# Kernel optimization log

Measured on AMD Instinct MI355X. Metric: run time of the kernel, lower is better.

Reference implementation:

```python
import jax, jax.numpy as jnp
import numpy as np

E = 1024      # embed_dim
H = 16        # num_heads
D = E // H    # head_dim = 64
K = 4         # num_hyper_nodes
MAX_SEQ = 8192
ROPE_BASE = 10000.0
SCALE = D ** -0.5


def rotate_half(x):
    half = x.shape[-1] // 2
    return jnp.concatenate([-x[..., half:], x[..., :half]], axis=-1)


def _rope_cache():
    inv_freq = 1.0 / (ROPE_BASE ** (jnp.arange(0, D, 2, dtype=jnp.float32) / D))
    t = jnp.arange(MAX_SEQ, dtype=jnp.float32)
    freqs = jnp.outer(t, inv_freq)                       # (MAX_SEQ, D/2)
    emb = jnp.concatenate([freqs, freqs], axis=-1)       # (MAX_SEQ, D)
    return jnp.cos(emb), jnp.sin(emb)


def setup_inputs() -> dict:
    key = jax.random.key(0)
    ks = jax.random.split(key, 6)
    B, S = 2, 2048
    w_scale = E ** -0.5  # keep pre-softmax logits in a sane range
    return {
        "x":  jax.random.normal(ks[0], (B, S, E), dtype=jnp.float32),
        "Wq": jax.random.normal(ks[1], (E, E), dtype=jnp.float32) * w_scale,
        "Wk": jax.random.normal(ks[2], (E, E), dtype=jnp.float32) * w_scale,
        "Wv": jax.random.normal(ks[3], (E, E), dtype=jnp.float32) * w_scale,
        "Wr": jax.random.normal(ks[4], (E, H * K), dtype=jnp.float32) * w_scale,
        "Wo": jax.random.normal(ks[5], (E, E), dtype=jnp.float32) * w_scale,
    }


def reference(x, Wq, Wk, Wv, Wr, Wo):
    B, S, _ = x.shape
    # projections -> (B, H, S, D)
    q = (x @ Wq).reshape(B, S, H, D).transpose(0, 2, 1, 3)
    k = (x @ Wk).reshape(B, S, H, D).transpose(0, 2, 1, 3)
    v = (x @ Wv).reshape(B, S, H, D).transpose(0, 2, 1, 3)

    # node routing probabilities (B, H, S, K)
    logits = (x @ Wr).reshape(B, S, H, K).transpose(0, 2, 1, 3)
    node_probs = jax.nn.softmax(logits, axis=-1)

    # expected per-node position: sum_{j<i} p[j,k]  -> (B, H, S, K)
    expected_pos = jnp.cumsum(node_probs, axis=2) - node_probs

    # fractional-position RoPE via linear interpolation of the cos/sin cache
    cos_c, sin_c = _rope_cache()
    pos = jnp.clip(expected_pos, 0.0, MAX_SEQ - 1)
    pf = pos.astype(jnp.int32)                   # floor
    pc = jnp.minimum(pf + 1, MAX_SEQ - 1)        # ceil
    frac = (pos - pf.astype(pos.dtype))[..., None]
    cos = cos_c[pf] + frac * (cos_c[pc] - cos_c[pf])   # (B,H,S,K,D)
    sin = sin_c[pf] + frac * (sin_c[pc] - sin_c[pf])

    # Weighted combine over nodes. Since q_k = q*cos_k + rh(q)*sin_k is linear
    # in (cos_k, sin_k), sum_k p_k * q_k = q * (sum_k p_k cos_k) + rh(q) * (sum_k p_k sin_k)
    cos_w = jnp.einsum('bhsk,bhskd->bhsd', node_probs, cos)
    sin_w = jnp.einsum('bhsk,bhskd->bhsd', node_probs, sin)
    q_r = q * cos_w + rotate_half(q) * sin_w
    k_r = k * cos_w + rotate_half(k) * sin_w

    # P(same node) weights (B, H, S, S)
    node_w = jnp.einsum('bhik,bhjk->bhij', node_probs, node_probs)

    scores = jnp.einsum('bhid,bhjd->bhij', q_r, k_r) * SCALE
    scores = scores + jnp.log(node_w + 1e-8)
    causal = jnp.tril(jnp.ones((S, S), dtype=bool))
    scores = jnp.where(causal[None, None], scores, -jnp.inf)
    attn = jax.nn.softmax(scores, axis=-1)

    out = jnp.einsum('bhij,bhjd->bhid', attn, v)
    out = out.transpose(0, 2, 1, 3).reshape(B, S, E)
    return out @ Wo
```

## Files before the change

### kernel.cpp

```cpp
#include <hip/hip_runtime.h>

#define E_ 1024
#define H_ 16
#define D_ 64
#define K_ 4
#define S_ 2048
#define B_ 2
#define BS_ 4096
#define BH_ 32
#define CT_ 2080

typedef __attribute__((ext_vector_type(8))) short short8;
typedef __attribute__((ext_vector_type(4))) float f32x4;
typedef __attribute__((ext_vector_type(4))) unsigned short u16x4;

__device__ __forceinline__ unsigned short f2bf(float f) {
  union { float f; unsigned u; } v; v.f = f;
  unsigned r = v.u + 0x7FFFu + ((v.u >> 16) & 1u);
  return (unsigned short)(r >> 16);
}
__device__ __forceinline__ float bf2f(unsigned short u) {
  union { unsigned u; float f; } v; v.u = ((unsigned)u) << 16; return v.f;
}

typedef __attribute__((address_space(1))) const void gvoid;
typedef __attribute__((address_space(3))) void lvoid;
__device__ __forceinline__ void gload_lds16(const void* g, void* l) {
  __builtin_amdgcn_global_load_lds((gvoid*)g, (lvoid*)l, 16, 0, 0);
}

__device__ __forceinline__ short8 lds8(const unsigned short* base, int row, int chunk) {
  int off = row * 128 + (((chunk ^ (row & 7)) & 7) << 4);
  return *(const short8*)((const char*)base + off);
}

#define SWZ_(d) (((d) & 7) ^ (((d) >> 3) & 7))

__global__ __launch_bounds__(256) void k_convert_x(const float* __restrict__ x,
                                                   unsigned short* __restrict__ xb) {
  int i = blockIdx.x * 256 + threadIdx.x;
  float4 v = ((const float4*)x)[i];
  u16x4 o; o.x = f2bf(v.x); o.y = f2bf(v.y); o.z = f2bf(v.z); o.w = f2bf(v.w);
  ((u16x4*)xb)[i] = o;
}

__global__ __launch_bounds__(256) void k_transpose_w(const float* __restrict__ Wq,
    const float* __restrict__ Wk, const float* __restrict__ Wv, const float* __restrict__ Wo,
    unsigned short* __restrict__ wt) {
  const float* W = blockIdx.z == 0 ? Wq : blockIdx.z == 1 ? Wk : blockIdx.z == 2 ? Wv : Wo;
  unsigned short* out = wt + (size_t)blockIdx.z * E_ * E_;
  __shared__ float tile[64][65];
  int k0 = blockIdx.y * 64, n0 = blockIdx.x * 64;
  int r = threadIdx.x >> 2, q4 = threadIdx.x & 3;
#pragma unroll
  for (int q = 0; q < 4; q++) {
    int c4 = q4 + q * 4;
    float4 v = *(const float4*)&W[(size_t)(k0 + r) * E_ + n0 + c4 * 4];
    tile[r][c4 * 4 + 0] = v.x; tile[r][c4 * 4 + 1] = v.y;
    tile[r][c4 * 4 + 2] = v.z; tile[r][c4 * 4 + 3] = v.w;
  }
  __syncthreads();
#pragma unroll
  for (int q = 0; q < 4; q++) {
    int cb = (q4 + q * 4) * 4;
    u16x4 o;
    o.x = f2bf(tile[cb + 0][r]); o.y = f2bf(tile[cb + 1][r]);
    o.z = f2bf(tile[cb + 2][r]); o.w = f2bf(tile[cb + 3][r]);
    *(u16x4*)&out[(size_t)(n0 + r) * E_ + k0 + cb] = o;
  }
}

__global__ __launch_bounds__(256) void k_cache(float* __restrict__ cosc, float* __restrict__ sinc) {
  int i = blockIdx.x * 256 + threadIdx.x;
  if (i >= CT_ * 32) return;
  int tt = i >> 5, f = i & 31;
  float invf = __expf(-(float)(2 * f) * (9.210340371976184f / 64.f));
  float ang = (float)tt * invf;
  cosc[i] = cosf(ang); sinc[i] = sinf(ang);
}

__global__ __launch_bounds__(256) void k_router(const float* __restrict__ x,
    const float* __restrict__ Wr, float* __restrict__ logits) {
  int rowblk = blockIdx.x * 8;
  int c = threadIdx.x & 63, rg = threadIdx.x >> 6;
  __shared__ float xs[8][128];
  float acc0 = 0.f, acc1 = 0.f;
  for (int e0 = 0; e0 < E_; e0 += 128) {
    __syncthreads();
    int idx = threadIdx.x;
    float4 v = *(const float4*)&x[(size_t)(rowblk + (idx >> 5)) * E_ + e0 + (idx & 31) * 4];
    *(float4*)&xs[idx >> 5][(idx & 31) * 4] = v;
    __syncthreads();
#pragma unroll 8
    for (int e = 0; e < 128; e++) {
      float w = Wr[(size_t)(e0 + e) * 64 + c];
      acc0 = fmaf(xs[rg * 2 + 0][e], w, acc0);
      acc1 = fmaf(xs[rg * 2 + 1][e], w, acc1);
    }
  }
  logits[(size_t)(rowblk + rg * 2 + 0) * 64 + c] = acc0;
  logits[(size_t)(rowblk + rg * 2 + 1) * 64 + c] = acc1;
}

__global__ __launch_bounds__(256) void k_scan(const float* __restrict__ logits,
    float* __restrict__ probs, unsigned short* __restrict__ pb, float* __restrict__ epos) {
  int bh = blockIdx.x; int b = bh >> 4, h = bh & 15;
  int t = threadIdx.x;
  float p[8][4];
  float own[4] = {0.f, 0.f, 0.f, 0.f};
#pragma unroll
  for (int r = 0; r < 8; r++) {
    int s = t * 8 + r;
    float4 lg = *(const float4*)&logits[(size_t)(b * S_ + s) * 64 + h * 4];
    float m = fmaxf(fmaxf(lg.x, lg.y), fmaxf(lg.z, lg.w));
    float e0 = __expf(lg.x - m), e1 = __expf(lg.y - m), e2 = __expf(lg.z - m), e3 = __expf(lg.w - m);
    float inv = 1.f / (e0 + e1 + e2 + e3);
    p[r][0] = e0 * inv; p[r][1] = e1 * inv; p[r][2] = e2 * inv; p[r][3] = e3 * inv;
    own[0] += p[r][0]; own[1] += p[r][1]; own[2] += p[r][2]; own[3] += p[r][3];
    float4 pv; pv.x = p[r][0]; pv.y = p[r][1]; pv.z = p[r][2]; pv.w = p[r][3];
    *(float4*)&probs[((size_t)bh * S_ + s) * 4] = pv;
    u16x4 pu; pu.x = f2bf(p[r][0]); pu.y = f2bf(p[r][1]);
    pu.z = f2bf(p[r][2]); pu.w = f2bf(p[r][3]);
    *(u16x4*)&pb[((size_t)bh * S_ + s) * 4] = pu;
  }
  __shared__ float sc[4][256];
#pragma unroll
  for (int k = 0; k < 4; k++) sc[k][t] = own[k];
  __syncthreads();
  for (int off = 1; off < 256; off <<= 1) {
    float v0 = 0, v1 = 0, v2 = 0, v3 = 0;
    if (t >= off) { v0 = sc[0][t - off]; v1 = sc[1][t - off]; v2 = sc[2][t - off]; v3 = sc[3][t - off]; }
    __syncthreads();
    if (t >= off) { sc[0][t] += v0; sc[1][t] += v1; sc[2][t] += v2; sc[3][t] += v3; }
    __syncthreads();
  }
  float run[4];
#pragma unroll
  for (int k = 0; k < 4; k++) run[k] = sc[k][t] - own[k];
#pragma unroll
  for (int r = 0; r < 8; r++) {
    int s = t * 8 + r;
    float4 ev; ev.x = run[0]; ev.y = run[1]; ev.z = run[2]; ev.w = run[3];
    *(float4*)&epos[((size_t)bh * S_ + s) * 4] = ev;
    run[0] += p[r][0]; run[1] += p[r][1]; run[2] += p[r][2]; run[3] += p[r][3];
  }
}

__global__ __launch_bounds__(256) void k_cwsw(const float* __restrict__ probs,
    const float* __restrict__ epos, const float* __restrict__ cosc, const float* __restrict__ sinc,
    float* __restrict__ cw, float* __restrict__ sw) {
  int bh = blockIdx.y;
  int s = blockIdx.x * 8 + (threadIdx.x >> 5);
  int f = threadIdx.x & 31;
  size_t row = (size_t)bh * S_ + s;
  float cacc = 0.f, sacc = 0.f;
#pragma unroll
  for (int k = 0; k < 4; k++) {
    float pk = probs[row * 4 + k];
    float pos = epos[row * 4 + k];
    pos = fminf(fmaxf(pos, 0.f), (float)(CT_ - 2));
    int pf = (int)pos; float fr = pos - (float)pf;
    float c0 = cosc[pf * 32 + f], c1 = cosc[pf * 32 + 32 + f];
    float s0 = sinc[pf * 32 + f], s1 = sinc[pf * 32 + 32 + f];
    cacc = fmaf(pk, c0 + fr * (c1 - c0), cacc);
    sacc = fmaf(pk, s0 + fr * (s1 - s0), sacc);
  }
  cw[row * 32 + f] = cacc; sw[row * 32 + f] = sacc;
}

__device__ __forceinline__ void gemm_128x128(const unsigned short* __restrict__ A,
    const unsigned short* __restrict__ Bt, int m0, int n0,
    unsigned short* lA, unsigned short* lB, f32x4 acc[4][4]) {
  int t = threadIdx.x, w = t >> 6, lane = t & 63;
  int wm = w >> 1, wn = w & 1;
  int arow = lane & 15, agrp = lane >> 4;
  for (int k0 = 0; k0 < E_; k0 += 64) {
    __syncthreads();
#pragma unroll
    for (int j = 0; j < 4; j++) {
      int c = j * 256 + w * 64 + lane;
      int row = c >> 3, slot = c & 7;
      gload_lds16(A + (size_t)(m0 + row) * E_ + k0 + ((slot ^ (row & 7)) << 3),
                  lA + (size_t)(j * 256 + w * 64) * 8);
      gload_lds16(Bt + (size_t)(n0 + row) * E_ + k0 + ((slot ^ (row & 7)) << 3),
                  lB + (size_t)(j * 256 + w * 64) * 8);
    }
    __syncthreads();
#pragma unroll
    for (int ks = 0; ks < 2; ks++) {
      short8 af[4], bfr[4];
#pragma unroll
      for (int mi = 0; mi < 4; mi++) af[mi] = lds8(lA, wm * 64 + mi * 16 + arow, ks * 4 + agrp);
#pragma unroll
      for (int nj = 0; nj < 4; nj++) bfr[nj] = lds8(lB, wn * 64 + nj * 16 + arow, ks * 4 + agrp);
#pragma unroll
      for (int mi = 0; mi < 4; mi++)
#pragma unroll
        for (int nj = 0; nj < 4; nj++)
          acc[mi][nj] = __builtin_amdgcn_mfma_f32_16x16x32_bf16(af[mi], bfr[nj], acc[mi][nj], 0, 0, 0);
    }
  }
}

__global__ __launch_bounds__(256) void k_gemm_qkv(const unsigned short* __restrict__ xb,
    const unsigned short* __restrict__ wt, const float* __restrict__ cw, const float* __restrict__ sw,
    unsigned short* __restrict__ qr, unsigned short* __restrict__ kr, unsigned short* __restrict__ vb) {
  __shared__ unsigned short lA[128 * 64], lB[128 * 64];
  int z = blockIdx.z;
  int m0 = blockIdx.y * 128, n0 = blockIdx.x * 128;
  f32x4 acc[4][4];
  f32x4 zero4 = {0.f, 0.f, 0.f, 0.f};
#pragma unroll
  for (int a = 0; a < 4; a++)
#pragma unroll
    for (int b2 = 0; b2 < 4; b2++) acc[a][b2] = zero4;
  gemm_128x128(xb, wt + (size_t)z * E_ * E_, m0, n0, lA, lB, acc);

  int t = threadIdx.x, w = t >> 6, lane = t & 63;
  int wm = w >> 1, wn = w & 1;
  int arow = lane & 15, agrp = lane >> 4;
  if (z == 2) {
#pragma unroll
    for (int mi = 0; mi < 4; mi++)
#pragma unroll
      for (int reg = 0; reg < 4; reg++) {
        int i = m0 + wm * 64 + mi * 16 + agrp * 4 + reg;
        int b = i >> 11, s = i & 2047;
#pragma unroll
        for (int nj = 0; nj < 4; nj++) {
          int col = n0 + wn * 64 + nj * 16 + arow;
          int h = col >> 6, d = col & 63;
          vb[((size_t)(b * H_ + h) * S_ + s) * 64 + d] = f2bf(acc[mi][nj][reg]);
        }
      }
  } else {
    unsigned short* out = (z == 0) ? qr : kr;
    float scl = (z == 0) ? 0.125f : 1.0f;
    int h = (n0 + wn * 64) >> 6;
#pragma unroll
    for (int mi = 0; mi < 4; mi++)
#pragma unroll
      for (int reg = 0; reg < 4; reg++) {
        int i = m0 + wm * 64 + mi * 16 + agrp * 4 + reg;
        int b = i >> 11, s = i & 2047;
        size_t rbase = (size_t)(b * H_ + h) * S_ + s;
        float cw0 = cw[rbase * 32 + arow], cw1 = cw[rbase * 32 + 16 + arow];
        float sw0 = sw[rbase * 32 + arow], sw1 = sw[rbase * 32 + 16 + arow];
#pragma unroll
        for (int nj = 0; nj < 4; nj++) {
          float v = acc[mi][nj][reg];
          float part = acc[mi][nj ^ 2][reg];
          float rh = (nj < 2) ? -part : part;
          float cwv = (nj & 1) ? cw1 : cw0;
          float swv = (nj & 1) ? sw1 : sw0;
          out[rbase * 64 + nj * 16 + arow] = f2bf((v * cwv + rh * swv) * scl);
        }
      }
  }
}

__global__ __launch_bounds__(256) void k_gemm_out(const unsigned short* __restrict__ ob,
    const unsigned short* __restrict__ wot, float* __restrict__ dout) {
  __shared__ unsigned short lA[64 * 64];
  __shared__ unsigned short lB[128 * 64];
  int m0 = blockIdx.y * 64, n0 = blockIdx.x * 128;
  int t = threadIdx.x, w = t >> 6, lane = t & 63;
  int arow = lane & 15, agrp = lane >> 4;
  f32x4 acc[4][2];
  f32x4 zero4 = {0.f, 0.f, 0.f, 0.f};
#pragma unroll
  for (int a = 0; a < 4; a++) { acc[a][0] = zero4; acc[a][1] = zero4; }
  for (int k0 = 0; k0 < E_; k0 += 64) {
    __syncthreads();
#pragma unroll
    for (int j = 0; j < 2; j++) {
      int c = j * 256 + t;
      int row = c >> 3, slot = c & 7;
      gload_lds16(ob + (size_t)(m0 + row) * E_ + k0 + ((slot ^ (row & 7)) << 3),
                  lA + (size_t)c * 8);
    }
#pragma unroll
    for (int j = 0; j < 4; j++) {
      int c = j * 256 + t;
      int row = c >> 3, slot = c & 7;
      gload_lds16(wot + (size_t)(n0 + row) * E_ + k0 + ((slot ^ (row & 7)) << 3),
                  lB + (size_t)c * 8);
    }
    __syncthreads();
#pragma unroll
    for (int ks = 0; ks < 2; ks++) {
      short8 af[4], bfr[2];
#pragma unroll
      for (int mi = 0; mi < 4; mi++) af[mi] = lds8(lA, mi * 16 + arow, ks * 4 + agrp);
#pragma unroll
      for (int nj = 0; nj < 2; nj++) bfr[nj] = lds8(lB, w * 32 + nj * 16 + arow, ks * 4 + agrp);
#pragma unroll
      for (int mi = 0; mi < 4; mi++)
#pragma unroll
        for (int nj = 0; nj < 2; nj++)
          acc[mi][nj] = __builtin_amdgcn_mfma_f32_16x16x32_bf16(af[mi], bfr[nj], acc[mi][nj], 0, 0, 0);
    }
  }
#pragma unroll
  for (int mi = 0; mi < 4; mi++)
#pragma unroll
    for (int reg = 0; reg < 4; reg++) {
      int i = m0 + mi * 16 + agrp * 4 + reg;
#pragma unroll
      for (int nj = 0; nj < 2; nj++) {
        int col = n0 + w * 32 + nj * 16 + arow;
        dout[(size_t)i * E_ + col] = acc[mi][nj][reg];
      }
    }
}

__device__ const int4 kChunk[38] = {
  { 8,0, 8, 8},{ 8,9,17, 9},{12,0, 8,19},{12,9,17,20},
  { 7,0, 7, 6},{ 7,8,15, 7},{10,0, 7,13},{11,0, 7,16},{11,8,15,17},{11,16,23,18},
  {12,18,25,21},{14,0, 7,26},{14,8,15,27},{15,0, 7,30},{15,8,15,31},{15,16,23,32},
  {15,24,31,33},{ 3,0, 7,-1},
  { 6,0, 6, 4},{ 6,7,13, 5},{ 9,0, 6,10},{ 9,7,13,11},{10,8,14,14},{10,15,21,15},
  {13,0, 6,22},{13,7,13,23},{13,14,20,24},{13,21,27,25},{14,16,22,28},{14,23,29,29},
  { 5,0, 5, 2},{ 5,6,11, 3},{ 9,14,19,12},{ 2,0, 5,-1},
  { 4,0, 4, 0},{ 4,5, 9, 1},{ 1,0, 3,-1},{ 0,0, 1,-1}
};

__device__ __forceinline__ void attn_half(
    const unsigned short* lK, unsigned short* lPh,
    const short8 piF, const short8 pjF[4],
    int kv0, int ig_base, int arow, int agrp,
    const short8 qf[2],
    float mrow[4], float lrow[4], f32x4 oacc[4]) {
  f32x4 zero4 = {0.f, 0.f, 0.f, 0.f};
  f32x4 eps4 = {1e-8f, 1e-8f, 1e-8f, 1e-8f};
  f32x4 sacc[4], nwa[4];
#pragma unroll
  for (int ct = 0; ct < 4; ct++) {
    sacc[ct] = zero4;
    nwa[ct] = __builtin_amdgcn_mfma_f32_16x16x32_bf16(piF, pjF[ct], eps4, 0, 0, 0);
  }
#pragma unroll
  for (int ks = 0; ks < 2; ks++) {
#pragma unroll
    for (int ct = 0; ct < 4; ct++) {
      short8 kf = lds8(lK, ct * 16 + arow, ks * 4 + agrp);
      sacc[ct] = __builtin_amdgcn_mfma_f32_16x16x32_bf16(qf[ks], kf, sacc[ct], 0, 0, 0);
    }
  }
  float sv[4][4];
  float rmax[4] = {-1e30f, -1e30f, -1e30f, -1e30f};
#pragma unroll
  for (int ct = 0; ct < 4; ct++) {
    int jg = kv0 + ct * 16 + arow;
#pragma unroll
    for (int reg = 0; reg < 4; reg++) {
      int ig = ig_base + agrp * 4 + reg;
      float xv = sacc[ct][reg];
      if (jg > ig) xv = -1e30f;
      sv[ct][reg] = xv;
      rmax[reg] = fmaxf(rmax[reg], xv);
    }
  }
#pragma unroll
  for (int reg = 0; reg < 4; reg++) {
    rmax[reg] = fmaxf(rmax[reg], __shfl_xor(rmax[reg], 1, 16));
    rmax[reg] = fmaxf(rmax[reg], __shfl_xor(rmax[reg], 2, 16));
    rmax[reg] = fmaxf(rmax[reg], __shfl_xor(rmax[reg], 4, 16));
    rmax[reg] = fmaxf(rmax[reg], __shfl_xor(rmax[reg], 8, 16));
  }
  float alpha[4], rsum[4];
#pragma unroll
  for (int reg = 0; reg < 4; reg++) {
    float mn = fmaxf(mrow[reg], rmax[reg]);
    alpha[reg] = __expf(mrow[reg] - mn);
    mrow[reg] = mn; rsum[reg] = 0.f;
  }
#pragma unroll
  for (int ct = 0; ct < 4; ct++)
#pragma unroll
    for (int reg = 0; reg < 4; reg++) {
      float p = __expf(sv[ct][reg] - mrow[reg]) * nwa[ct][reg];
      sv[ct][reg] = p; rsum[reg] += p;
    }
#pragma unroll
  for (int reg = 0; reg < 4; reg++) {
    rsum[reg] += __shfl_xor(rsum[reg], 1, 16);
    rsum[reg] += __shfl_xor(rsum[reg], 2, 16);
    rsum[reg] += __shfl_xor(rsum[reg], 4, 16);
    rsum[reg] += __shfl_xor(rsum[reg], 8, 16);
    lrow[reg] = lrow[reg] * alpha[reg] + rsum[reg];
  }
#pragma unroll
  for (int dt = 0; dt < 4; dt++) {
    f32x4 o = oacc[dt];
    o.x *= alpha[0]; o.y *= alpha[1]; o.z *= alpha[2]; o.w *= alpha[3];
    oacc[dt] = o;
  }
#pragma unroll
  for (int ct = 0; ct < 4; ct++)
#pragma unroll
    for (int reg = 0; reg < 4; reg++) {
      int row = agrp * 4 + reg, col = ct * 16 + arow;
      int off = row * 128 + ((col * 2) ^ ((row & 7) << 4));
      *(unsigned short*)((char*)lPh + off) = f2bf(sv[ct][reg]);
    }
}

__device__ __forceinline__ void attn_pv(const unsigned short* lPh, const unsigned short* lV,
    int arow, int agrp, f32x4 oacc[4]) {
#pragma unroll
  for (int ks = 0; ks < 2; ks++) {
    short8 pf8 = lds8(lPh, arow, ks * 4 + agrp);
#pragma unroll
    for (int dt = 0; dt < 4; dt++) {
      int d = dt * 16 + arow;
      int off = d * 128 + ((((ks * 4 + agrp)) ^ SWZ_(d)) << 4);
      short8 vf = *(const short8*)((char*)lV + off);
      oacc[dt] = __builtin_amdgcn_mfma_f32_16x16x32_bf16(pf8, vf, oacc[dt], 0, 0, 0);
    }
  }
}

__global__ __launch_bounds__(256, 2) void k_attn(const unsigned short* __restrict__ qr,
    const unsigned short* __restrict__ kr, const unsigned short* __restrict__ vb,
    const unsigned short* __restrict__ pb, unsigned short* __restrict__ ob,
    unsigned short* __restrict__ ObP, float* __restrict__ ml) {
  __shared__ unsigned short lK[64 * 64];
  __shared__ unsigned short lV[64 * 64];
  __shared__ unsigned short lP[4][2][16 * 64];
  int4 ck = kChunk[blockIdx.x];
  int qt2 = ck.x, j0 = ck.y, j1 = ck.z, part = ck.w;
  int bh = blockIdx.y;
  int t = threadIdx.x, w = t >> 6, lane = t & 63;
  int arow = lane & 15, agrp = lane >> 4;
  int q0 = qt2 * 128;
  size_t base = (size_t)bh * S_ * 64;
  size_t bhS = (size_t)bh * S_;

  short8 qf[2][2];
  short8 piF[2];
  float mrow[2][4], lrow[2][4];
  f32x4 oacc[2][4];
  f32x4 zero4 = {0.f, 0.f, 0.f, 0.f};
#pragma unroll
  for (int hh = 0; hh < 2; hh++) {
#pragma unroll
    for (int ks = 0; ks < 2; ks++)
      qf[hh][ks] = *(const short8*)&qr[base + (size_t)(q0 + hh * 64 + w * 16 + arow) * 64 + ks * 32 + agrp * 8];
    short8 z = {0, 0, 0, 0, 0, 0, 0, 0};
    if (agrp == 0) {
      u16x4 pv = *(const u16x4*)&pb[(bhS + q0 + hh * 64 + w * 16 + arow) * 4];
      z[0] = (short)pv.x; z[1] = (short)pv.y; z[2] = (short)pv.z; z[3] = (short)pv.w;
    }
    piF[hh] = z;
#pragma unroll
    for (int reg = 0; reg < 4; reg++) { mrow[hh][reg] = -1e30f; lrow[hh][reg] = 0.f; }
#pragma unroll
    for (int dt = 0; dt < 4; dt++) oacc[hh][dt] = zero4;
  }

  for (int jt = j0; jt <= j1; jt++) {
    int kv0 = jt * 64;
    __syncthreads();
#pragma unroll
    for (int j = 0; j < 2; j++) {
      int c = j * 256 + w * 64 + lane;
      int row = c >> 3, slot = c & 7;
      gload_lds16(kr + base + (size_t)(kv0 + row) * 64 + ((slot ^ (row & 7)) << 3),
                  lK + (size_t)(j * 256 + w * 64) * 8);
    }
#pragma unroll
    for (int j = 0; j < 2; j++) {
      int c = j * 256 + t;
      int row = c >> 3; int d0 = (c & 7) * 8;
      short8 vv = *(const short8*)&vb[base + (size_t)(kv0 + row) * 64 + d0];
#pragma unroll
      for (int x = 0; x < 8; x++) {
        int d = d0 + x;
        int off = d * 128 + ((row * 2) ^ (SWZ_(d) << 4));
        *(unsigned short*)((char*)lV + off) = (unsigned short)vv[x];
      }
    }
    short8 pjF[4];
#pragma unroll
    for (int ct = 0; ct < 4; ct++) {
      short8 z = {0, 0, 0, 0, 0, 0, 0, 0};
      if (agrp == 0) {
        u16x4 pv = *(const u16x4*)&pb[(bhS + kv0 + ct * 16 + arow) * 4];
        z[0] = (short)pv.x; z[1] = (short)pv.y; z[2] = (short)pv.z; z[3] = (short)pv.w;
      }
      pjF[ct] = z;
    }
    __syncthreads();

    __builtin_amdgcn_s_setprio(1);
#pragma unroll
    for (int hh = 0; hh < 2; hh++)
      attn_half(lK, &lP[w][hh][0], piF[hh], pjF, kv0, q0 + hh * 64 + w * 16, arow, agrp,
                qf[hh], mrow[hh], lrow[hh], oacc[hh]);
    __builtin_amdgcn_s_setprio(0);
    asm volatile("s_waitcnt lgkmcnt(0)" ::: "memory");
    __builtin_amdgcn_sched_barrier(0);
    __builtin_amdgcn_s_setprio(1);
#pragma unroll
    for (int hh = 0; hh < 2; hh++)
      attn_pv(&lP[w][hh][0], lV, arow, agrp, oacc[hh]);
    __builtin_amdgcn_s_setprio(0);
  }

  if (part >= 0) {
    unsigned short* Op = ObP + ((size_t)bh * 34 + part) * 8192;
    float* mlp = ml + ((size_t)bh * 34 + part) * 256;
#pragma unroll
    for (int hh = 0; hh < 2; hh++) {
#pragma unroll
      for (int dt = 0; dt < 4; dt++)
#pragma unroll
        for (int reg = 0; reg < 4; reg++) {
          int row = hh * 64 + w * 16 + agrp * 4 + reg;
          Op[row * 64 + dt * 16 + arow] = f2bf(oacc[hh][dt][reg]);
        }
      if (arow == 0) {
#pragma unroll
        for (int reg = 0; reg < 4; reg++) {
          int row = hh * 64 + w * 16 + agrp * 4 + reg;
          mlp[row] = mrow[hh][reg];
          mlp[128 + row] = lrow[hh][reg];
        }
      }
    }
  } else {
    int b = bh >> 4, h8 = bh & 15;
#pragma unroll
    for (int hh = 0; hh < 2; hh++)
#pragma unroll
      for (int dt = 0; dt < 4; dt++)
#pragma unroll
        for (int reg = 0; reg < 4; reg++) {
          int i = q0 + hh * 64 + w * 16 + agrp * 4 + reg;
          int d = dt * 16 + arow;
          float v = oacc[hh][dt][reg] / lrow[hh][reg];
          ob[((size_t)(b * S_ + i) * H_ + h8) * 64 + d] = f2bf(v);
        }
  }
}

__global__ __launch_bounds__(256) void k_merge(const unsigned short* __restrict__ ObP,
    const float* __restrict__ ml, unsigned short* __restrict__ ob) {
  int qx = blockIdx.x, bh = blockIdx.y;
  int qt2 = 4 + qx;
  int np = qt2 <= 8 ? 2 : (qt2 <= 12 ? 3 : 4);
  int bslot = qt2 <= 8 ? (qt2 - 4) * 2 : (qt2 <= 12 ? 10 + (qt2 - 9) * 3 : 22 + (qt2 - 13) * 4);
  int t = threadIdx.x;
  int r = t >> 1, dh = (t & 1) * 32;
  float mp[4], lp[4];
  float m = -1e30f;
  for (int p2 = 0; p2 < np; p2++) {
    const float* mlp = ml + ((size_t)bh * 34 + bslot + p2) * 256;
    mp[p2] = mlp[r]; lp[p2] = mlp[128 + r];
    m = fmaxf(m, mp[p2]);
  }
  float a[4], l = 0.f;
  for (int p2 = 0; p2 < np; p2++) { a[p2] = __expf(mp[p2] - m); l = fmaf(lp[p2], a[p2], l); }
  float inv = 1.f / l;
  for (int p2 = 0; p2 < np; p2++) a[p2] *= inv;
  int i = qt2 * 128 + r, b = bh >> 4, h = bh & 15;
  unsigned short* op = ob + ((size_t)(b * S_ + i) * H_ + h) * 64 + dh;
#pragma unroll
  for (int q = 0; q < 8; q++) {
    float a0 = 0.f, a1 = 0.f, a2 = 0.f, a3 = 0.f;
    for (int p2 = 0; p2 < np; p2++) {
      const unsigned short* Op = ObP + ((size_t)bh * 34 + bslot + p2) * 8192 + r * 64 + dh + q * 4;
      u16x4 xx = *(const u16x4*)Op;
      a0 = fmaf(bf2f(xx.x), a[p2], a0);
      a1 = fmaf(bf2f(xx.y), a[p2], a1);
      a2 = fmaf(bf2f(xx.z), a[p2], a2);
      a3 = fmaf(bf2f(xx.w), a[p2], a3);
    }
    u16x4 o; o.x = f2bf(a0); o.y = f2bf(a1); o.z = f2bf(a2); o.w = f2bf(a3);
    *(u16x4*)(op + q * 4) = o;
  }
}

extern "C" void kernel_launch(void* const* d_in, const int* in_sizes, int n_in,
                              void* d_out, int out_size, void* d_ws, size_t ws_size,
                              hipStream_t stream) {
  const float* x  = (const float*)d_in[0];
  const float* Wq = (const float*)d_in[1];
  const float* Wk = (const float*)d_in[2];
  const float* Wv = (const float*)d_in[3];
  const float* Wr = (const float*)d_in[4];
  const float* Wo = (const float*)d_in[5];
  float* dout = (float*)d_out;

  char* p = (char*)d_ws;
  auto alloc = [&](size_t bytes) -> char* {
    char* r = p; p += (bytes + 255) & ~(size_t)255; return r;
  };
  unsigned short* xb   = (unsigned short*)alloc((size_t)BS_ * E_ * 2);
  unsigned short* wt   = (unsigned short*)alloc((size_t)4 * E_ * E_ * 2);
  float* cosc          = (float*)alloc((size_t)CT_ * 32 * 4);
  float* sinc          = (float*)alloc((size_t)CT_ * 32 * 4);
  float* probs         = (float*)alloc((size_t)BH_ * S_ * 4 * 4);
  unsigned short* pb   = (unsigned short*)alloc((size_t)BH_ * S_ * 4 * 2);
  float* logits        = (float*)alloc((size_t)BS_ * 64 * 4);
  float* epos          = (float*)alloc((size_t)BH_ * S_ * 4 * 4);
  float* cw            = (float*)alloc((size_t)BH_ * S_ * 32 * 4);
  float* sw            = (float*)alloc((size_t)BH_ * S_ * 32 * 4);
  unsigned short* qrb  = (unsigned short*)alloc((size_t)BH_ * S_ * 64 * 2);
  unsigned short* krb  = (unsigned short*)alloc((size_t)BH_ * S_ * 64 * 2);
  unsigned short* vbb  = (unsigned short*)alloc((size_t)BH_ * S_ * 64 * 2);
  unsigned short* obb  = (unsigned short*)alloc((size_t)BS_ * E_ * 2);
  if ((size_t)(p - (char*)d_ws) > ws_size) return;

  unsigned short* ObP = (unsigned short*)logits;
  float* mlbuf = (float*)xb;

  k_convert_x<<<BS_ * E_ / 4 / 256, 256, 0, stream>>>(x, xb);
  k_transpose_w<<<dim3(16, 16, 4), 256, 0, stream>>>(Wq, Wk, Wv, Wo, wt);
  k_cache<<<(CT_ * 32 + 255) / 256, 256, 0, stream>>>(cosc, sinc);
  k_router<<<BS_ / 8, 256, 0, stream>>>(x, Wr, logits);
  k_scan<<<BH_, 256, 0, stream>>>(logits, probs, pb, epos);
  k_cwsw<<<dim3(S_ / 8, BH_), 256, 0, stream>>>(probs, epos, cosc, sinc, cw, sw);
  k_gemm_qkv<<<dim3(8, 32, 3), 256, 0, stream>>>(xb, wt, cw, sw, qrb, krb, vbb);
  k_attn<<<dim3(38, BH_), 256, 0, stream>>>(qrb, krb, vbb, pb, obb, ObP, mlbuf);
  k_merge<<<dim3(12, BH_), 256, 0, stream>>>(ObP, mlbuf, obb);
  k_gemm_out<<<dim3(8, 64), 256, 0, stream>>>(obb, wt + (size_t)3 * E_ * E_, dout);
}
```

Before: 230.6 us.

## Double-buffer K/V tiles in attention, use exp2 softmax, remap blocks per XCD

The attention kernel now double-buffers K and V in LDS and prefetches the next tile's K, V and routing probabilities while the current tile is processed. This leaves one barrier per iteration and overlaps global loads with MFMA work. The QK and PV MFMAs for both query halves are interleaved to share K/V fragment loads, and the causal mask is skipped on tiles that lie fully below the diagonal. Softmax switches to exp2 with log2(e) folded into the Q scale. The 2D grid is flattened and remapped so each XCD handles a fixed set of heads for L2 locality. These changes double LDS use and add register pressure, which may lower occupancy.

```diff
diff --git a/kernel.cpp b/kernel.cpp
--- a/kernel.cpp
+++ b/kernel.cpp
@@ -235,7 +235,7 @@
       }
   } else {
     unsigned short* out = (z == 0) ? qr : kr;
-    float scl = (z == 0) ? 0.125f : 1.0f;
+    float scl = (z == 0) ? 0.18033688011f : 1.0f;
     int h = (n0 + wn * 64) >> 6;
 #pragma unroll
     for (int mi = 0; mi < 4; mi++)
@@ -325,41 +325,50 @@
   { 4,0, 4, 0},{ 4,5, 9, 1},{ 1,0, 3,-1},{ 0,0, 1,-1}
 };
 
-__device__ __forceinline__ void attn_half(
-    const unsigned short* lK, unsigned short* lPh,
-    const short8 piF, const short8 pjF[4],
-    int kv0, int ig_base, int arow, int agrp,
-    const short8 qf[2],
+__device__ __forceinline__ void qk_phase(const unsigned short* lKc, const short8 qf[2][2],
+                                         int arow, int agrp, f32x4 sacc[2][4]) {
+#pragma unroll
+  for (int ks = 0; ks < 2; ks++)
+#pragma unroll
+    for (int ct = 0; ct < 4; ct++) {
+      short8 kf = lds8(lKc, ct * 16 + arow, ks * 4 + agrp);
+      sacc[0][ct] = __builtin_amdgcn_mfma_f32_16x16x32_bf16(qf[0][ks], kf, sacc[0][ct], 0, 0, 0);
+      sacc[1][ct] = __builtin_amdgcn_mfma_f32_16x16x32_bf16(qf[1][ks], kf, sacc[1][ct], 0, 0, 0);
+    }
+}
+
+__device__ __forceinline__ void softmax_half(const f32x4 sacc[4], const short8 piF,
+    const short8 pjF[4], unsigned short* lPh, int kv0, int ig_base, int arow, int agrp,
     float mrow[4], float lrow[4], f32x4 oacc[4]) {
-  f32x4 zero4 = {0.f, 0.f, 0.f, 0.f};
   f32x4 eps4 = {1e-8f, 1e-8f, 1e-8f, 1e-8f};
-  f32x4 sacc[4], nwa[4];
-#pragma unroll
-  for (int ct = 0; ct < 4; ct++) {
-    sacc[ct] = zero4;
+  f32x4 nwa[4];
+#pragma unroll
+  for (int ct = 0; ct < 4; ct++)
     nwa[ct] = __builtin_amdgcn_mfma_f32_16x16x32_bf16(piF, pjF[ct], eps4, 0, 0, 0);
-  }
-#pragma unroll
-  for (int ks = 0; ks < 2; ks++) {
-#pragma unroll
-    for (int ct = 0; ct < 4; ct++) {
-      short8 kf = lds8(lK, ct * 16 + arow, ks * 4 + agrp);
-      sacc[ct] = __builtin_amdgcn_mfma_f32_16x16x32_bf16(qf[ks], kf, sacc[ct], 0, 0, 0);
-    }
-  }
   float sv[4][4];
   float rmax[4] = {-1e30f, -1e30f, -1e30f, -1e30f};
-#pragma unroll
-  for (int ct = 0; ct < 4; ct++) {
-    int jg = kv0 + ct * 16 + arow;
-#pragma unroll
-    for (int reg = 0; reg < 4; reg++) {
-      int ig = ig_base + agrp * 4 + reg;
-      float xv = sacc[ct][reg];
-      if (jg > ig) xv = -1e30f;
-      sv[ct][reg] = xv;
-      rmax[reg] = fmaxf(rmax[reg], xv);
-    }
+  if (kv0 + 63 > ig_base) {
+#pragma unroll
+    for (int ct = 0; ct < 4; ct++) {
+      int jg = kv0 + ct * 16 + arow;
+#pragma unroll
+      for (int reg = 0; reg < 4; reg++) {
+        int ig = ig_base + agrp * 4 + reg;
+        float xv = sacc[ct][reg];
+        if (jg > ig) xv = -1e30f;
+        sv[ct][reg] = xv;
+        rmax[reg] = fmaxf(rmax[reg], xv);
+      }
+    }
+  } else {
+#pragma unroll
+    for (int ct = 0; ct < 4; ct++)
+#pragma unroll
+      for (int reg = 0; reg < 4; reg++) {
+        float xv = sacc[ct][reg];
+        sv[ct][reg] = xv;
+        rmax[reg] = fmaxf(rmax[reg], xv);
+      }
   }
 #pragma unroll
   for (int reg = 0; reg < 4; reg++) {
@@ -372,14 +381,14 @@
 #pragma unroll
   for (int reg = 0; reg < 4; reg++) {
     float mn = fmaxf(mrow[reg], rmax[reg]);
-    alpha[reg] = __expf(mrow[reg] - mn);
+    alpha[reg] = __builtin_amdgcn_exp2f(mrow[reg] - mn);
     mrow[reg] = mn; rsum[reg] = 0.f;
   }
 #pragma unroll
   for (int ct = 0; ct < 4; ct++)
 #pragma unroll
     for (int reg = 0; reg < 4; reg++) {
-      float p = __expf(sv[ct][reg] - mrow[reg]) * nwa[ct][reg];
+      float p = __builtin_amdgcn_exp2f(sv[ct][reg] - mrow[reg]) * nwa[ct][reg];
       sv[ct][reg] = p; rsum[reg] += p;
     }
 #pragma unroll
@@ -406,17 +415,19 @@
     }
 }
 
-__device__ __forceinline__ void attn_pv(const unsigned short* lPh, const unsigned short* lV,
-    int arow, int agrp, f32x4 oacc[4]) {
+__device__ __forceinline__ void pv_phase(const unsigned short* lP0, const unsigned short* lP1,
+    const unsigned short* lVc, int arow, int agrp, f32x4 oacc0[4], f32x4 oacc1[4]) {
 #pragma unroll
   for (int ks = 0; ks < 2; ks++) {
-    short8 pf8 = lds8(lPh, arow, ks * 4 + agrp);
+    short8 pf0 = lds8(lP0, arow, ks * 4 + agrp);
+    short8 pf1 = lds8(lP1, arow, ks * 4 + agrp);
 #pragma unroll
     for (int dt = 0; dt < 4; dt++) {
       int d = dt * 16 + arow;
       int off = d * 128 + ((((ks * 4 + agrp)) ^ SWZ_(d)) << 4);
-      short8 vf = *(const short8*)((char*)lV + off);
-      oacc[dt] = __builtin_amdgcn_mfma_f32_16x16x32_bf16(pf8, vf, oacc[dt], 0, 0, 0);
+      short8 vf = *(const short8*)((const char*)lVc + off);
+      oacc0[dt] = __builtin_amdgcn_mfma_f32_16x16x32_bf16(pf0, vf, oacc0[dt], 0, 0, 0);
+      oacc1[dt] = __builtin_amdgcn_mfma_f32_16x16x32_bf16(pf1, vf, oacc1[dt], 0, 0, 0);
     }
   }
 }
@@ -425,12 +436,14 @@
     const unsigned short* __restrict__ kr, const unsigned short* __restrict__ vb,
     const unsigned short* __restrict__ pb, unsigned short* __restrict__ ob,
     unsigned short* __restrict__ ObP, float* __restrict__ ml) {
-  __shared__ unsigned short lK[64 * 64];
-  __shared__ unsigned short lV[64 * 64];
+  __shared__ unsigned short lK[2][64 * 64];
+  __shared__ unsigned short lV[2][64 * 64];
   __shared__ unsigned short lP[4][2][16 * 64];
-  int4 ck = kChunk[blockIdx.x];
+  int id = blockIdx.x;
+  int xcd = id & 7, slt = id >> 3;
+  int bh = xcd * 4 + (slt & 3);
+  int4 ck = kChunk[slt >> 2];
   int qt2 = ck.x, j0 = ck.y, j1 = ck.z, part = ck.w;
-  int bh = blockIdx.y;
   int t = threadIdx.x, w = t >> 6, lane = t & 63;
   int arow = lane & 15, agrp = lane >> 4;
   int q0 = qt2 * 128;
@@ -447,11 +460,10 @@
 #pragma unroll
     for (int ks = 0; ks < 2; ks++)
       qf[hh][ks] = *(const short8*)&qr[base + (size_t)(q0 + hh * 64 + w * 16 + arow) * 64 + ks * 32 + agrp * 8];
+    u16x4 pv = {0, 0, 0, 0};
+    if (agrp == 0) pv = *(const u16x4*)&pb[(bhS + q0 + hh * 64 + w * 16 + arow) * 4];
     short8 z = {0, 0, 0, 0, 0, 0, 0, 0};
-    if (agrp == 0) {
-      u16x4 pv = *(const u16x4*)&pb[(bhS + q0 + hh * 64 + w * 16 + arow) * 4];
-      z[0] = (short)pv.x; z[1] = (short)pv.y; z[2] = (short)pv.z; z[3] = (short)pv.w;
-    }
+    z[0] = (short)pv.x; z[1] = (short)pv.y; z[2] = (short)pv.z; z[3] = (short)pv.w;
     piF[hh] = z;
 #pragma unroll
     for (int reg = 0; reg < 4; reg++) { mrow[hh][reg] = -1e30f; lrow[hh][reg] = 0.f; }
@@ -459,53 +471,101 @@
     for (int dt = 0; dt < 4; dt++) oacc[hh][dt] = zero4;
   }
 
-  for (int jt = j0; jt <= j1; jt++) {
-    int kv0 = jt * 64;
-    __syncthreads();
+  auto stageK = [&](int jt, int buf) {
 #pragma unroll
     for (int j = 0; j < 2; j++) {
       int c = j * 256 + w * 64 + lane;
       int row = c >> 3, slot = c & 7;
-      gload_lds16(kr + base + (size_t)(kv0 + row) * 64 + ((slot ^ (row & 7)) << 3),
-                  lK + (size_t)(j * 256 + w * 64) * 8);
-    }
+      gload_lds16(kr + base + (size_t)(jt * 64 + row) * 64 + ((slot ^ (row & 7)) << 3),
+                  &lK[buf][(size_t)(j * 256 + w * 64) * 8]);
+    }
+  };
+  auto loadV = [&](int jt, short8 vr[2]) {
 #pragma unroll
     for (int j = 0; j < 2; j++) {
       int c = j * 256 + t;
-      int row = c >> 3; int d0 = (c & 7) * 8;
-      short8 vv = *(const short8*)&vb[base + (size_t)(kv0 + row) * 64 + d0];
+      int row = c >> 3, d0 = (c & 7) * 8;
+      vr[j] = *(const short8*)&vb[base + (size_t)(jt * 64 + row) * 64 + d0];
+    }
+  };
+  auto scatterV = [&](const short8 vr[2], int buf) {
+#pragma unroll
+    for (int j = 0; j < 2; j++) {
+      int c = j * 256 + t;
+      int row = c >> 3, d0 = (c & 7) * 8;
 #pragma unroll
       for (int x = 0; x < 8; x++) {
         int d = d0 + x;
         int off = d * 128 + ((row * 2) ^ (SWZ_(d) << 4));
-        *(unsigned short*)((char*)lV + off) = (unsigned short)vv[x];
+        *(unsigned short*)((char*)&lV[buf][0] + off) = (unsigned short)vr[j][x];
       }
     }
+  };
+  auto loadPj = [&](int jt, u16x4 pj[4]) {
+#pragma unroll
+    for (int ct = 0; ct < 4; ct++) {
+      u16x4 z = {0, 0, 0, 0};
+      if (agrp == 0) z = *(const u16x4*)&pb[(bhS + jt * 64 + ct * 16 + arow) * 4];
+      pj[ct] = z;
+    }
+  };
+
+  short8 vreg[2];
+  u16x4 pjv[4], pjvn[4];
+  loadV(j0, vreg);
+  stageK(j0, 0);
+  scatterV(vreg, 0);
+  loadPj(j0, pjv);
+  __syncthreads();
+
+  int nt = j1 - j0 + 1;
+  for (int i = 0; i < nt; i++) {
+    int cur = i & 1;
+    int kv0 = (j0 + i) * 64;
+    bool hn = (i + 1) < nt;
+    if (hn) {
+      loadV(j0 + i + 1, vreg);
+      stageK(j0 + i + 1, cur ^ 1);
+    }
+
+    f32x4 sacc[2][4];
+#pragma unroll
+    for (int hh = 0; hh < 2; hh++)
+#pragma unroll
+      for (int ct = 0; ct < 4; ct++) sacc[hh][ct] = zero4;
+
+    __builtin_amdgcn_s_setprio(1);
+    qk_phase(&lK[cur][0], qf, arow, agrp, sacc);
+    __builtin_amdgcn_s_setprio(0);
+
     short8 pjF[4];
 #pragma unroll
     for (int ct = 0; ct < 4; ct++) {
       short8 z = {0, 0, 0, 0, 0, 0, 0, 0};
-      if (agrp == 0) {
-        u16x4 pv = *(const u16x4*)&pb[(bhS + kv0 + ct * 16 + arow) * 4];
-        z[0] = (short)pv.x; z[1] = (short)pv.y; z[2] = (short)pv.z; z[3] = (short)pv.w;
-      }
+      z[0] = (short)pjv[ct].x; z[1] = (short)pjv[ct].y;
+      z[2] = (short)pjv[ct].z; z[3] = (short)pjv[ct].w;
       pjF[ct] = z;
     }
-    __syncthreads();
-
-    __builtin_amdgcn_s_setprio(1);
 #pragma unroll
     for (int hh = 0; hh < 2; hh++)
-      attn_half(lK, &lP[w][hh][0], piF[hh], pjF, kv0, q0 + hh * 64 + w * 16, arow, agrp,
-                qf[hh], mrow[hh], lrow[hh], oacc[hh]);
-    __builtin_amdgcn_s_setprio(0);
+      softmax_half(sacc[hh], piF[hh], pjF, &lP[w][hh][0], kv0, q0 + hh * 64 + w * 16,
+                   arow, agrp, mrow[hh], lrow[hh], oacc[hh]);
+
+    if (hn) {
+      scatterV(vreg, cur ^ 1);
+      loadPj(j0 + i + 1, pjvn);
+    }
+
     asm volatile("s_waitcnt lgkmcnt(0)" ::: "memory");
     __builtin_amdgcn_sched_barrier(0);
     __builtin_amdgcn_s_setprio(1);
-#pragma unroll
-    for (int hh = 0; hh < 2; hh++)
-      attn_pv(&lP[w][hh][0], lV, arow, agrp, oacc[hh]);
+    pv_phase(&lP[w][0][0], &lP[w][1][0], &lV[cur][0], arow, agrp, oacc[0], oacc[1]);
     __builtin_amdgcn_s_setprio(0);
+    if (hn) {
+#pragma unroll
+      for (int ct = 0; ct < 4; ct++) pjv[ct] = pjvn[ct];
+    }
+    __syncthreads();
   }
 
   if (part >= 0) {
@@ -561,7 +621,7 @@
     m = fmaxf(m, mp[p2]);
   }
   float a[4], l = 0.f;
-  for (int p2 = 0; p2 < np; p2++) { a[p2] = __expf(mp[p2] - m); l = fmaf(lp[p2], a[p2], l); }
+  for (int p2 = 0; p2 < np; p2++) { a[p2] = __builtin_amdgcn_exp2f(mp[p2] - m); l = fmaf(lp[p2], a[p2], l); }
   float inv = 1.f / l;
   for (int p2 = 0; p2 < np; p2++) a[p2] *= inv;
   int i = qt2 * 128 + r, b = bh >> 4, h = bh & 15;
@@ -623,7 +683,7 @@
   k_scan<<<BH_, 256, 0, stream>>>(logits, probs, pb, epos);
   k_cwsw<<<dim3(S_ / 8, BH_), 256, 0, stream>>>(probs, epos, cosc, sinc, cw, sw);
   k_gemm_qkv<<<dim3(8, 32, 3), 256, 0, stream>>>(xb, wt, cw, sw, qrb, krb, vbb);
-  k_attn<<<dim3(38, BH_), 256, 0, stream>>>(qrb, krb, vbb, pb, obb, ObP, mlbuf);
+  k_attn<<<dim3(38 * BH_), 256, 0, stream>>>(qrb, krb, vbb, pb, obb, ObP, mlbuf);
   k_merge<<<dim3(12, BH_), 256, 0, stream>>>(ObP, mlbuf, obb);
   k_gemm_out<<<dim3(8, 64), 256, 0, stream>>>(obb, wt + (size_t)3 * E_ * E_, dout);
 }
```

Measured after the change: 224.1 us. 2.8% less time.
